# Performance work log

Measured on AMD Instinct MI355X. Metric: run time of the kernel, lower is better.

## Reference

```python
import jax, jax.numpy as jnp
import numpy as np

HIDDEN = 2048
NUM_HEADS = 16
NUM_KV_HEADS = 4
HEAD_DIM = HIDDEN // NUM_HEADS  # 128
GROUP = NUM_HEADS // NUM_KV_HEADS  # 4
SCALE = HEAD_DIM ** -0.5


def setup_inputs() -> dict:
    key = jax.random.key(0)
    ks = jax.random.split(key, 9)
    B, S = 2, 2048
    kv_dim = HEAD_DIM * NUM_KV_HEADS
    std = HIDDEN ** -0.5
    return {
        "x": jax.random.normal(ks[0], (B, S, HIDDEN), dtype=jnp.float32),
        "Wq": jax.random.normal(ks[1], (HIDDEN, HIDDEN), dtype=jnp.float32) * std,
        "bq": jnp.zeros((HIDDEN,), dtype=jnp.float32),
        "Wk": jax.random.normal(ks[2], (HIDDEN, kv_dim), dtype=jnp.float32) * std,
        "bk": jnp.zeros((kv_dim,), dtype=jnp.float32),
        "Wv": jax.random.normal(ks[3], (HIDDEN, kv_dim), dtype=jnp.float32) * std,
        "bv": jnp.zeros((kv_dim,), dtype=jnp.float32),
        "Wo": jax.random.normal(ks[4], (HIDDEN, HIDDEN), dtype=jnp.float32) * std,
        "bo": jnp.zeros((HIDDEN,), dtype=jnp.float32),
    }


def reference(x, Wq, bq, Wk, bk, Wv, bv, Wo, bo):
    B, S, _ = x.shape
    # projections
    q = (x @ Wq + bq).reshape(B, S, NUM_KV_HEADS, GROUP, HEAD_DIM)  # grouped query heads
    k = (x @ Wk + bk).reshape(B, S, NUM_KV_HEADS, HEAD_DIM)
    v = (x @ Wv + bv).reshape(B, S, NUM_KV_HEADS, HEAD_DIM)
    # scores: [B, Hkv, G, Sq, Sk] -- same math as repeat_interleave of K/V over G,
    # but K/V are broadcast over the group axis instead of materialized.
    attn = jnp.einsum("bqhgd,bkhd->bhgqk", q, k) * SCALE
    attn = jax.nn.softmax(attn, axis=-1)
    out = jnp.einsum("bhgqk,bkhd->bqhgd", attn, v).reshape(B, S, HIDDEN)
    return out @ Wo + bo
```

## Files before the change

### kernel.cpp

```cpp
#include <hip/hip_runtime.h>


#define SEQ    2048
#define HIDDEN 2048

typedef __attribute__((ext_vector_type(8))) short v8s;
typedef __attribute__((ext_vector_type(4))) float v4f;

#define MFMA16(a,b,c) __builtin_amdgcn_mfma_f32_16x16x32_bf16((a),(b),(c),0,0,0)

__device__ __forceinline__ ushort f2b(float f){
  unsigned u = __float_as_uint(f);
  u += 0x7fffu + ((u >> 16) & 1u);
  return (ushort)(u >> 16);
}

__device__ __forceinline__ void gload16(const void* g, void* l){
  __builtin_amdgcn_global_load_lds((const __attribute__((address_space(1))) void*)g,
                                   (__attribute__((address_space(3))) void*)l, 16, 0, 0);
}

#define WAIT_VM0   0x0F70
#define WAIT_LGKM0 0xC07F

__global__ void k_conv(const float* __restrict__ in, ushort* __restrict__ out, int n){
  int i = (blockIdx.x*256 + threadIdx.x)*4;
  if (i >= n) return;
  float4 f = *(const float4*)(in + i);
  ushort4 u; u.x=f2b(f.x); u.y=f2b(f.y); u.z=f2b(f.z); u.w=f2b(f.w);
  *(ushort4*)(out + i) = u;
}

__global__ void k_tconv(const float* __restrict__ in, ushort* __restrict__ out,
                        int rows, int cols){
  __shared__ float t[32][33];
  int tx = threadIdx.x & 31, ty = threadIdx.x >> 5;
  int c0 = blockIdx.x*32, r0 = blockIdx.y*32;
#pragma unroll
  for (int i=0;i<4;i++) t[ty+i*8][tx] = in[(size_t)(r0+ty+i*8)*cols + c0+tx];
  __syncthreads();
#pragma unroll
  for (int i=0;i<4;i++) out[(size_t)(c0+ty+i*8)*rows + r0+tx] = f2b(t[tx][ty+i*8]);
}

__global__ void k_tv(const ushort* __restrict__ vb, ushort* __restrict__ vT){
  __shared__ ushort t[32][33];
  int tx = threadIdx.x & 31, ty = threadIdx.x >> 5;
  int s0 = blockIdx.x*32, d0 = blockIdx.y*32, bh = blockIdx.z;
  int b = bh >> 2, h = bh & 3;
  const ushort* src = vb + (size_t)b*SEQ*512 + h*128;
#pragma unroll
  for (int i=0;i<4;i++) t[ty+i*8][tx] = src[(size_t)(s0+ty+i*8)*512 + d0+tx];
  __syncthreads();
  ushort* dst = vT + (size_t)bh*128*SEQ;
#pragma unroll
  for (int i=0;i<4;i++) dst[(size_t)(d0+ty+i*8)*SEQ + s0+tx] = t[tx][ty+i*8];
}

#define GEMM_MAIN(A_, Bt_, K_)                                                        \
  __shared__ ushort sA[128*32], sB[128*32];                                           \
  const int tid = threadIdx.x, lane = tid & 63, wid = tid >> 6;                       \
  const int wm = wid >> 1, wn = wid & 1, lm = lane & 15, q8 = (lane >> 4)*8;          \
  const int rowB = blockIdx.y*128, colB = blockIdx.x*128;                             \
  v4f acc[4][4] = {};                                                                 \
  for (int k0 = 0; k0 < (K_); k0 += 32){                                              \
    _Pragma("unroll")                                                                 \
    for (int it=0; it<2; it++){                                                       \
      int c = tid + it*256;                                                           \
      gload16((A_)  + (size_t)(rowB + (c>>2))*(K_) + k0 + (c&3)*8, (char*)sA + c*16); \
      gload16((Bt_) + (size_t)(colB + (c>>2))*(K_) + k0 + (c&3)*8, (char*)sB + c*16); \
    }                                                                                 \
    __syncthreads();                                                                  \
    v8s af[4], bfr[4];                                                                \
    _Pragma("unroll")                                                                 \
    for (int i=0;i<4;i++){                                                            \
      af[i]  = *(const v8s*)(sA + (wm*64 + i*16 + lm)*32 + q8);                       \
      bfr[i] = *(const v8s*)(sB + (wn*64 + i*16 + lm)*32 + q8);                       \
    }                                                                                 \
    _Pragma("unroll")                                                                 \
    for (int i=0;i<4;i++)                                                             \
      _Pragma("unroll")                                                               \
      for (int j=0;j<4;j++) acc[i][j] = MFMA16(af[i], bfr[j], acc[i][j]);             \
    __syncthreads();                                                                  \
  }                                                                                   \
  const int quad = lane >> 4;

__global__ __launch_bounds__(256) void k_gemm_qkv(
    const ushort* __restrict__ A, const ushort* __restrict__ Bt,
    const float* __restrict__ bq, const float* __restrict__ bk, const float* __restrict__ bv,
    ushort* __restrict__ qb, ushort* __restrict__ kb, ushort* __restrict__ vb){
  GEMM_MAIN(A, Bt, HIDDEN)
#pragma unroll
  for (int i=0;i<4;i++)
#pragma unroll
  for (int j=0;j<4;j++){
    int col = colB + wn*64 + j*16 + lm;
#pragma unroll
    for (int r=0;r<4;r++){
      int row = rowB + wm*64 + i*16 + quad*4 + r;
      float v = acc[i][j][r];
      if (col < 2048)      qb[(size_t)row*2048 + col]        = f2b(v + bq[col]);
      else if (col < 2560) kb[(size_t)row*512 + (col-2048)]  = f2b(v + bk[col-2048]);
      else                 vb[(size_t)row*512 + (col-2560)]  = f2b(v + bv[col-2560]);
    }
  }
}

__global__ __launch_bounds__(256) void k_gemm_out(
    const ushort* __restrict__ A, const ushort* __restrict__ Bt,
    const float* __restrict__ bo, float* __restrict__ out){
  GEMM_MAIN(A, Bt, HIDDEN)
#pragma unroll
  for (int i=0;i<4;i++)
#pragma unroll
  for (int j=0;j<4;j++){
    int col = colB + wn*64 + j*16 + lm;
#pragma unroll
    for (int r=0;r<4;r++){
      int row = rowB + wm*64 + i*16 + quad*4 + r;
      out[(size_t)row*2048 + col] = acc[i][j][r] + bo[col];
    }
  }
}

__global__ __launch_bounds__(256, 1) void k_attn(
    const ushort* __restrict__ qb, const ushort* __restrict__ kb,
    const ushort* __restrict__ vT, ushort* __restrict__ Ob){
  __shared__ ushort sK[2][64*128];
  __shared__ ushort sV[2][128*64];
  __shared__ ushort sP[4][4096];
  const int tid = threadIdx.x, lane = tid & 63, w = tid >> 6;
  const int lm = lane & 15, quad = lane >> 4, q8 = quad*8;
  const int pair = blockIdx.x & 7;
  const int hkv = pair & 3, b = pair >> 2;
  const int qt = (blockIdx.x >> 3) & 7, g = blockIdx.x >> 6;
  const int head = hkv*4 + g;
  const float C = 0.08838834764831845f * 1.4426950408889634f;

  const ushort* kbb = kb + (size_t)b*SEQ*512 + hkv*128;
  const ushort* vbb = vT + (size_t)(b*4+hkv)*128*SEQ;

  const int kk = lane >> 4, ksw = lane & 15;
  const int dd = lane >> 3, vsw = lane & 7;

#define STAGE_K(t, buf) { _Pragma("unroll") for (int i=0;i<4;i++){                     \
    int c = w*4 + i; int key = c*4 + kk; int wd = ksw ^ (key & 15);                    \
    gload16(kbb + (size_t)((t)*64 + key)*512 + wd*8, &sK[buf][c*512 + lane*8]); } }
#define STAGE_V(t, buf) { _Pragma("unroll") for (int i=0;i<4;i++){                     \
    int c = w*4 + i; int drow = c*8 + dd; int wd = vsw ^ dd;                           \
    gload16(vbb + (size_t)drow*SEQ + (t)*64 + wd*8, &sV[buf][c*512 + lane*8]); } }

  v8s qf[4][4];
#pragma unroll
  for (int rb=0; rb<4; rb++)
#pragma unroll
    for (int ks=0; ks<4; ks++)
      qf[rb][ks] = *(const v8s*)(qb + (size_t)(b*SEQ + qt*256 + w*64 + rb*16 + lm)*HIDDEN
                                    + head*128 + ks*32 + q8);

  v4f o[4][8] = {};
  float lreg[4] = {0.f, 0.f, 0.f, 0.f};

  STAGE_K(0, 0)
  STAGE_V(0, 0)
  __builtin_amdgcn_s_waitcnt(WAIT_VM0);
  __syncthreads();

  for (int t=0; t<32; t++){
    const int cur = t & 1;
    if (t < 31) STAGE_K(t+1, cur^1)

    v8s kf[4][4];
#pragma unroll
    for (int kt=0; kt<4; kt++)
#pragma unroll
      for (int ks=0; ks<4; ks++)
        kf[kt][ks] = *(const v8s*)(&sK[cur][(kt*16+lm)*128 + ((ks*4+quad)^lm)*8]);

    v4f sacc[4][4] = {};
#pragma unroll
    for (int ks=0; ks<4; ks++)
#pragma unroll
      for (int kt=0; kt<4; kt++)
#pragma unroll
        for (int rb=0; rb<4; rb++)
          sacc[rb][kt] = MFMA16(kf[kt][ks], qf[rb][ks], sacc[rb][kt]);

#pragma unroll
    for (int rb=0; rb<4; rb++){
      float rs = 0.f;
#pragma unroll
      for (int kt=0; kt<4; kt++){
        float p0 = __builtin_amdgcn_exp2f(sacc[rb][kt][0]*C);
        float p1 = __builtin_amdgcn_exp2f(sacc[rb][kt][1]*C);
        float p2 = __builtin_amdgcn_exp2f(sacc[rb][kt][2]*C);
        float p3 = __builtin_amdgcn_exp2f(sacc[rb][kt][3]*C);
        rs += (p0+p1)+(p2+p3);
        uint2 pk;
        pk.x = (unsigned)f2b(p0) | ((unsigned)f2b(p1) << 16);
        pk.y = (unsigned)f2b(p2) | ((unsigned)f2b(p3) << 16);
        int kc = kt >> 1;
        int dl = ((kt&1)*2 + (quad>>1))*16 + lm;
        *(uint2*)(&sP[w][(rb*2+kc)*512 + dl*8 + (quad&1)*4]) = pk;
      }
      lreg[rb] += rs;
    }

    __builtin_amdgcn_s_waitcnt(WAIT_VM0);
    __syncthreads();
    if (t < 31) STAGE_V(t+1, cur^1)

    __builtin_amdgcn_s_waitcnt(WAIT_LGKM0);
    v8s pa[4][2];
#pragma unroll
    for (int rb=0; rb<4; rb++)
#pragma unroll
      for (int kc=0; kc<2; kc++)
        pa[rb][kc] = *(const v8s*)(&sP[w][(rb*2+kc)*512 + lane*8]);
    v8s vf[8][2];
#pragma unroll
    for (int dt=0; dt<8; dt++)
#pragma unroll
      for (int kc=0; kc<2; kc++)
        vf[dt][kc] = *(const v8s*)(&sV[cur][(dt*16+lm)*64 + ((kc*4+quad)^(lm&7))*8]);
#pragma unroll
    for (int kc=0; kc<2; kc++)
#pragma unroll
      for (int dt=0; dt<8; dt++)
#pragma unroll
        for (int rb=0; rb<4; rb++)
          o[rb][dt] = MFMA16(pa[rb][kc], vf[dt][kc], o[rb][dt]);
  }

#pragma unroll
  for (int rb=0; rb<4; rb++){
    float lv = lreg[rb];
    lv += __shfl_xor(lv, 16);
    lv += __shfl_xor(lv, 32);
    float inv[4];
#pragma unroll
    for (int r=0;r<4;r++) inv[r] = 1.0f / __shfl(lv, (lane & 48) + quad*4 + r);
#pragma unroll
    for (int dt=0; dt<8; dt++)
#pragma unroll
      for (int r=0;r<4;r++){
        int row = b*SEQ + qt*256 + w*64 + rb*16 + quad*4 + r;
        int col = head*128 + dt*16 + lm;
        Ob[(size_t)row*HIDDEN + col] = f2b(o[rb][dt][r]*inv[r]);
      }
  }
#undef STAGE_K
#undef STAGE_V
}

extern "C" void kernel_launch(void* const* d_in, const int* in_sizes, int n_in,
                              void* d_out, int out_size, void* d_ws, size_t ws_size,
                              hipStream_t stream){
  const float* x  = (const float*)d_in[0];
  const float* Wq = (const float*)d_in[1];
  const float* bq = (const float*)d_in[2];
  const float* Wk = (const float*)d_in[3];
  const float* bk = (const float*)d_in[4];
  const float* Wv = (const float*)d_in[5];
  const float* bv = (const float*)d_in[6];
  const float* Wo = (const float*)d_in[7];
  const float* bo = (const float*)d_in[8];
  float* out = (float*)d_out;

  ushort* xb  = (ushort*)d_ws;
  ushort* Wt  = xb  + 8388608;
  ushort* Wto = Wt  + 6291456;
  ushort* qb  = Wto + 4194304;
  ushort* kb  = qb  + 8388608;
  ushort* vb  = kb  + 2097152;
  ushort* vT  = vb  + 2097152;
  ushort* Ob  = vT  + 2097152;

  k_conv <<<8192, 256, 0, stream>>>(x, xb, 8388608);
  k_tconv<<<dim3(64,64), 256, 0, stream>>>(Wq, Wt, 2048, 2048);
  k_tconv<<<dim3(16,64), 256, 0, stream>>>(Wk, Wt + 4194304, 2048, 512);
  k_tconv<<<dim3(16,64), 256, 0, stream>>>(Wv, Wt + 5242880, 2048, 512);
  k_tconv<<<dim3(64,64), 256, 0, stream>>>(Wo, Wto, 2048, 2048);
  k_gemm_qkv<<<dim3(24,32), 256, 0, stream>>>(xb, Wt, bq, bk, bv, qb, kb, vb);
  k_tv  <<<dim3(64,4,8), 256, 0, stream>>>(vb, vT);
  k_attn<<<256, 256, 0, stream>>>(qb, kb, vT, Ob);
  k_gemm_out<<<dim3(16,32), 256, 0, stream>>>(Ob, Wto, bo, out);
}
```

Baseline: 351.6 us.

## Halve attention query tile, pass P via shuffles, widen GEMM K-step with swizzle

The attention kernel now gives each wave 32 query rows instead of 64 and launches 512 blocks with two blocks per CU allowed. The P matrix is rearranged into MFMA A-operand layout with cross-lane shuffles rather than a round trip through shared memory, and the V prefetch is issued together with the K prefetch. The shared GEMM main loop now loads 64-wide K slices into XOR-swizzled shared memory, which halves the number of barriers and avoids LDS bank conflicts. The aim is better latency hiding and fewer sync points, at the cost of extra shuffle instructions and K/V being reloaded for twice as many blocks.

```diff
diff --git a/kernel.cpp b/kernel.cpp
--- a/kernel.cpp
+++ b/kernel.cpp
@@ -21,7 +21,6 @@
 }
 
 #define WAIT_VM0   0x0F70
-#define WAIT_LGKM0 0xC07F
 
 __global__ void k_conv(const float* __restrict__ in, ushort* __restrict__ out, int n){
   int i = (blockIdx.x*256 + threadIdx.x)*4;
@@ -58,32 +57,34 @@
 }
 
 #define GEMM_MAIN(A_, Bt_, K_)                                                        \
-  __shared__ ushort sA[128*32], sB[128*32];                                           \
+  __shared__ ushort sA[128*64], sB[128*64];                                           \
   const int tid = threadIdx.x, lane = tid & 63, wid = tid >> 6;                       \
-  const int wm = wid >> 1, wn = wid & 1, lm = lane & 15, q8 = (lane >> 4)*8;          \
+  const int wm = wid >> 1, wn = wid & 1, lm = lane & 15, quad = lane >> 4;            \
   const int rowB = blockIdx.y*128, colB = blockIdx.x*128;                             \
   v4f acc[4][4] = {};                                                                 \
-  for (int k0 = 0; k0 < (K_); k0 += 32){                                              \
+  for (int k0 = 0; k0 < (K_); k0 += 64){                                              \
     _Pragma("unroll")                                                                 \
-    for (int it=0; it<2; it++){                                                       \
-      int c = tid + it*256;                                                           \
-      gload16((A_)  + (size_t)(rowB + (c>>2))*(K_) + k0 + (c&3)*8, (char*)sA + c*16); \
-      gload16((Bt_) + (size_t)(colB + (c>>2))*(K_) + k0 + (c&3)*8, (char*)sB + c*16); \
+    for (int it=0; it<4; it++){                                                       \
+      int c = tid + it*256; int row = c>>3, wg = (c&7)^(row&7);                       \
+      gload16((A_)  + (size_t)(rowB+row)*(K_) + k0 + wg*8, (char*)sA + c*16);         \
+      gload16((Bt_) + (size_t)(colB+row)*(K_) + k0 + wg*8, (char*)sB + c*16);         \
     }                                                                                 \
     __syncthreads();                                                                  \
-    v8s af[4], bfr[4];                                                                \
     _Pragma("unroll")                                                                 \
-    for (int i=0;i<4;i++){                                                            \
-      af[i]  = *(const v8s*)(sA + (wm*64 + i*16 + lm)*32 + q8);                       \
-      bfr[i] = *(const v8s*)(sB + (wn*64 + i*16 + lm)*32 + q8);                       \
+    for (int ks=0; ks<2; ks++){                                                       \
+      v8s af[4], bfr[4];                                                              \
+      _Pragma("unroll")                                                               \
+      for (int i=0;i<4;i++){                                                          \
+        af[i]  = *(const v8s*)(sA + (wm*64+i*16+lm)*64 + ((ks*4+quad)^(lm&7))*8);     \
+        bfr[i] = *(const v8s*)(sB + (wn*64+i*16+lm)*64 + ((ks*4+quad)^(lm&7))*8);     \
+      }                                                                               \
+      _Pragma("unroll")                                                               \
+      for (int i=0;i<4;i++)                                                           \
+        _Pragma("unroll")                                                             \
+        for (int j=0;j<4;j++) acc[i][j] = MFMA16(af[i], bfr[j], acc[i][j]);           \
     }                                                                                 \
-    _Pragma("unroll")                                                                 \
-    for (int i=0;i<4;i++)                                                             \
-      _Pragma("unroll")                                                               \
-      for (int j=0;j<4;j++) acc[i][j] = MFMA16(af[i], bfr[j], acc[i][j]);             \
     __syncthreads();                                                                  \
-  }                                                                                   \
-  const int quad = lane >> 4;
+  }
 
 __global__ __launch_bounds__(256) void k_gemm_qkv(
     const ushort* __restrict__ A, const ushort* __restrict__ Bt,
@@ -123,17 +124,16 @@
   }
 }
 
-__global__ __launch_bounds__(256, 1) void k_attn(
+__global__ __launch_bounds__(256, 2) void k_attn(
     const ushort* __restrict__ qb, const ushort* __restrict__ kb,
     const ushort* __restrict__ vT, ushort* __restrict__ Ob){
   __shared__ ushort sK[2][64*128];
   __shared__ ushort sV[2][128*64];
-  __shared__ ushort sP[4][4096];
   const int tid = threadIdx.x, lane = tid & 63, w = tid >> 6;
   const int lm = lane & 15, quad = lane >> 4, q8 = quad*8;
   const int pair = blockIdx.x & 7;
   const int hkv = pair & 3, b = pair >> 2;
-  const int qt = (blockIdx.x >> 3) & 7, g = blockIdx.x >> 6;
+  const int qt = (blockIdx.x >> 3) & 15, g = blockIdx.x >> 7;
   const int head = hkv*4 + g;
   const float C = 0.08838834764831845f * 1.4426950408889634f;
 
@@ -150,16 +150,16 @@
     int c = w*4 + i; int drow = c*8 + dd; int wd = vsw ^ dd;                           \
     gload16(vbb + (size_t)drow*SEQ + (t)*64 + wd*8, &sV[buf][c*512 + lane*8]); } }
 
-  v8s qf[4][4];
-#pragma unroll
-  for (int rb=0; rb<4; rb++)
+  v8s qf[2][4];
+#pragma unroll
+  for (int rb=0; rb<2; rb++)
 #pragma unroll
     for (int ks=0; ks<4; ks++)
-      qf[rb][ks] = *(const v8s*)(qb + (size_t)(b*SEQ + qt*256 + w*64 + rb*16 + lm)*HIDDEN
+      qf[rb][ks] = *(const v8s*)(qb + (size_t)(b*SEQ + qt*128 + w*32 + rb*16 + lm)*HIDDEN
                                     + head*128 + ks*32 + q8);
 
-  v4f o[4][8] = {};
-  float lreg[4] = {0.f, 0.f, 0.f, 0.f};
+  v4f o[2][8] = {};
+  float lreg[2] = {0.f, 0.f};
 
   STAGE_K(0, 0)
   STAGE_V(0, 0)
@@ -168,26 +168,25 @@
 
   for (int t=0; t<32; t++){
     const int cur = t & 1;
-    if (t < 31) STAGE_K(t+1, cur^1)
-
-    v8s kf[4][4];
-#pragma unroll
-    for (int kt=0; kt<4; kt++)
+    if (t < 31){ STAGE_K(t+1, cur^1) STAGE_V(t+1, cur^1) }
+
+    v4f sacc[2][4] = {};
+#pragma unroll
+    for (int kt=0; kt<4; kt++){
+      v8s kf[4];
 #pragma unroll
       for (int ks=0; ks<4; ks++)
-        kf[kt][ks] = *(const v8s*)(&sK[cur][(kt*16+lm)*128 + ((ks*4+quad)^lm)*8]);
-
-    v4f sacc[4][4] = {};
-#pragma unroll
-    for (int ks=0; ks<4; ks++)
-#pragma unroll
-      for (int kt=0; kt<4; kt++)
-#pragma unroll
-        for (int rb=0; rb<4; rb++)
-          sacc[rb][kt] = MFMA16(kf[kt][ks], qf[rb][ks], sacc[rb][kt]);
-
-#pragma unroll
-    for (int rb=0; rb<4; rb++){
+        kf[ks] = *(const v8s*)(&sK[cur][(kt*16+lm)*128 + ((ks*4+quad)^lm)*8]);
+#pragma unroll
+      for (int ks=0; ks<4; ks++)
+#pragma unroll
+        for (int rb=0; rb<2; rb++)
+          sacc[rb][kt] = MFMA16(kf[ks], qf[rb][ks], sacc[rb][kt]);
+    }
+
+    uint2 pk[2][4];
+#pragma unroll
+    for (int rb=0; rb<2; rb++){
       float rs = 0.f;
 #pragma unroll
       for (int kt=0; kt<4; kt++){
@@ -196,44 +195,52 @@
         float p2 = __builtin_amdgcn_exp2f(sacc[rb][kt][2]*C);
         float p3 = __builtin_amdgcn_exp2f(sacc[rb][kt][3]*C);
         rs += (p0+p1)+(p2+p3);
-        uint2 pk;
-        pk.x = (unsigned)f2b(p0) | ((unsigned)f2b(p1) << 16);
-        pk.y = (unsigned)f2b(p2) | ((unsigned)f2b(p3) << 16);
-        int kc = kt >> 1;
-        int dl = ((kt&1)*2 + (quad>>1))*16 + lm;
-        *(uint2*)(&sP[w][(rb*2+kc)*512 + dl*8 + (quad&1)*4]) = pk;
+        pk[rb][kt].x = (unsigned)f2b(p0) | ((unsigned)f2b(p1) << 16);
+        pk[rb][kt].y = (unsigned)f2b(p2) | ((unsigned)f2b(p3) << 16);
       }
       lreg[rb] += rs;
     }
 
+    const int slo = ((quad & 1) << 5) + lm;
+    const bool hi = (quad >> 1) != 0;
+    v8s pa[2][2];
+#pragma unroll
+    for (int rb=0; rb<2; rb++)
+#pragma unroll
+      for (int kc=0; kc<2; kc++){
+        union { uint u[4]; v8s s; } pu;
+        unsigned ax = __shfl((int)pk[rb][2*kc].x,   slo);
+        unsigned ay = __shfl((int)pk[rb][2*kc].y,   slo);
+        unsigned bx = __shfl((int)pk[rb][2*kc+1].x, slo);
+        unsigned by = __shfl((int)pk[rb][2*kc+1].y, slo);
+        unsigned cx = __shfl((int)pk[rb][2*kc].x,   slo+16);
+        unsigned cy = __shfl((int)pk[rb][2*kc].y,   slo+16);
+        unsigned dx = __shfl((int)pk[rb][2*kc+1].x, slo+16);
+        unsigned dy = __shfl((int)pk[rb][2*kc+1].y, slo+16);
+        pu.u[0] = hi ? bx : ax;  pu.u[1] = hi ? by : ay;
+        pu.u[2] = hi ? dx : cx;  pu.u[3] = hi ? dy : cy;
+        pa[rb][kc] = pu.s;
+      }
+
+#pragma unroll
+    for (int dt=0; dt<8; dt++){
+      v8s vf[2];
+#pragma unroll
+      for (int kc=0; kc<2; kc++)
+        vf[kc] = *(const v8s*)(&sV[cur][(dt*16+lm)*64 + ((kc*4+quad)^(lm&7))*8]);
+#pragma unroll
+      for (int kc=0; kc<2; kc++)
+#pragma unroll
+        for (int rb=0; rb<2; rb++)
+          o[rb][dt] = MFMA16(pa[rb][kc], vf[kc], o[rb][dt]);
+    }
+
     __builtin_amdgcn_s_waitcnt(WAIT_VM0);
     __syncthreads();
-    if (t < 31) STAGE_V(t+1, cur^1)
-
-    __builtin_amdgcn_s_waitcnt(WAIT_LGKM0);
-    v8s pa[4][2];
-#pragma unroll
-    for (int rb=0; rb<4; rb++)
-#pragma unroll
-      for (int kc=0; kc<2; kc++)
-        pa[rb][kc] = *(const v8s*)(&sP[w][(rb*2+kc)*512 + lane*8]);
-    v8s vf[8][2];
-#pragma unroll
-    for (int dt=0; dt<8; dt++)
-#pragma unroll
-      for (int kc=0; kc<2; kc++)
-        vf[dt][kc] = *(const v8s*)(&sV[cur][(dt*16+lm)*64 + ((kc*4+quad)^(lm&7))*8]);
-#pragma unroll
-    for (int kc=0; kc<2; kc++)
-#pragma unroll
-      for (int dt=0; dt<8; dt++)
-#pragma unroll
-        for (int rb=0; rb<4; rb++)
-          o[rb][dt] = MFMA16(pa[rb][kc], vf[dt][kc], o[rb][dt]);
-  }
-
-#pragma unroll
-  for (int rb=0; rb<4; rb++){
+  }
+
+#pragma unroll
+  for (int rb=0; rb<2; rb++){
     float lv = lreg[rb];
     lv += __shfl_xor(lv, 16);
     lv += __shfl_xor(lv, 32);
@@ -244,7 +251,7 @@
     for (int dt=0; dt<8; dt++)
 #pragma unroll
       for (int r=0;r<4;r++){
-        int row = b*SEQ + qt*256 + w*64 + rb*16 + quad*4 + r;
+        int row = b*SEQ + qt*128 + w*32 + rb*16 + quad*4 + r;
         int col = head*128 + dt*16 + lm;
         Ob[(size_t)row*HIDDEN + col] = f2b(o[rb][dt][r]*inv[r]);
       }
@@ -283,6 +290,6 @@
   k_tconv<<<dim3(64,64), 256, 0, stream>>>(Wo, Wto, 2048, 2048);
   k_gemm_qkv<<<dim3(24,32), 256, 0, stream>>>(xb, Wt, bq, bk, bv, qb, kb, vb);
   k_tv  <<<dim3(64,4,8), 256, 0, stream>>>(vb, vT);
-  k_attn<<<256, 256, 0, stream>>>(qb, kb, vT, Ob);
+  k_attn<<<512, 256, 0, stream>>>(qb, kb, vT, Ob);
   k_gemm_out<<<dim3(16,32), 256, 0, stream>>>(Ob, Wto, bo, out);
 }
```

Measured after the change: 355.0 us. No clear change (+1.0%).
